# Kernel optimization log

Measured on AMD Instinct MI355X. Metric: run time of the kernel, lower is better.

## Reference

```python
import jax, jax.numpy as jnp
import numpy as np

N = 50000      # nodes
E = 800000     # edges (avg degree 16)
D_IN, D_H, D_OUT = 128, 128, 64


def setup_inputs() -> dict:
    key = jax.random.key(0)
    ks = jax.random.split(key, 12)
    s = 0.05  # weight init scale
    return {
        "x": jax.random.normal(ks[0], (N, D_IN), jnp.float32),
        "edge_index": jax.random.randint(ks[1], (2, E), 0, N, dtype=jnp.int64),
        "Wl0": jax.random.normal(ks[2], (D_H, D_IN), jnp.float32) * s,
        "bl0": jax.random.normal(ks[3], (D_H,), jnp.float32) * s,
        "Wr0": jax.random.normal(ks[4], (D_H, D_IN), jnp.float32) * s,
        "Wl1": jax.random.normal(ks[5], (D_H, D_H), jnp.float32) * s,
        "bl1": jax.random.normal(ks[6], (D_H,), jnp.float32) * s,
        "Wr1": jax.random.normal(ks[7], (D_H, D_H), jnp.float32) * s,
        "Wl2": jax.random.normal(ks[8], (D_OUT, D_H), jnp.float32) * s,
        "bl2": jax.random.normal(ks[9], (D_OUT,), jnp.float32) * s,
        "Wr2": jax.random.normal(ks[10], (D_OUT, D_H), jnp.float32) * s,
    }


def _sage_layer(h, src, dst, Wl, bl, Wr):
    # mean aggregation over incoming neighbors: out[i] = mean_{j in N(i)} h[j]
    n = h.shape[0]
    agg = jax.ops.segment_sum(h[src], dst, num_segments=n)          # [N, D]
    deg = jax.ops.segment_sum(jnp.ones((src.shape[0],), h.dtype), dst,
                              num_segments=n)                        # [N]
    mean = agg / jnp.maximum(deg, 1.0)[:, None]  # empty rows -> 0, matches torch_sparse
    # lin_l(agg) + lin_r(self); lin_r has no bias in PyG SAGEConv
    return mean @ Wl.T + bl + h @ Wr.T


def reference(x, edge_index, Wl0, bl0, Wr0, Wl1, bl1, Wr1, Wl2, bl2, Wr2):
    src, dst = edge_index[1], edge_index[0]  # adj row = dst, col = src
    h = jax.nn.relu(_sage_layer(x, src, dst, Wl0, bl0, Wr0))
    h = jax.nn.relu(_sage_layer(h, src, dst, Wl1, bl1, Wr1))
    h = _sage_layer(h, src, dst, Wl2, bl2, Wr2)
    return jax.nn.log_softmax(h, axis=1)
```

## Files before the change

kernel.cpp:

```cpp
#include <hip/hip_runtime.h>
#include <hip/hip_bf16.h>


typedef __attribute__((ext_vector_type(8))) short bf16x8;
typedef __attribute__((ext_vector_type(4))) float f32x4;

#define NPB 128
#define BCAP 2560
#define EPB 8192
#define EPT 32
#define CPAD 16

__device__ __forceinline__ unsigned short f2bf(float f) {
    unsigned int u = __builtin_bit_cast(unsigned int, f);
    u += 0x7fffu + ((u >> 16) & 1u);
    return (unsigned short)(u >> 16);
}
__device__ __forceinline__ float bf2f(unsigned int bits16) {
    return __builtin_bit_cast(float, bits16 << 16);
}


__global__ __launch_bounds__(256) void dist_cast_kernel(
        const int* __restrict__ dst, const int* __restrict__ srcv,
        int* __restrict__ gcnt, unsigned int* __restrict__ staging, int E, int NBc,
        const float* __restrict__ x,
        const float* p0, const float* p1, const float* p2,
        const float* p3, const float* p4, const float* p5,
        unsigned short* __restrict__ xbf, unsigned short* __restrict__ wbf,
        int xpairs, int distBlocks) {
    __shared__ unsigned int stage[EPB];
    __shared__ int hist[400];
    __shared__ int lstart[400];
    __shared__ int gbase[400];
    __shared__ int scanbuf[256];
    int t = threadIdx.x;

    if (blockIdx.x >= distBlocks) {
        int bid = blockIdx.x - distBlocks;
        int xblocks = (xpairs + 255) / 256;
        if (bid < xblocks) {
            int i = bid * 256 + t;
            if (i < xpairs) {
                float2 v = ((const float2*)x)[i];
                unsigned int p = (unsigned int)f2bf(v.x) | ((unsigned int)f2bf(v.y) << 16);
                ((unsigned int*)xbf)[i] = p;
            }
        } else {
            int w = (bid - xblocks) * 256 + t;
            if (w < 40960) {
                const float* src;
                int local;
                if      (w < 8192)  { src = p0; local = w; }
                else if (w < 16384) { src = p1; local = w - 8192; }
                else if (w < 24576) { src = p2; local = w - 16384; }
                else if (w < 32768) { src = p3; local = w - 24576; }
                else if (w < 36864) { src = p4; local = w - 32768; }
                else                { src = p5; local = w - 36864; }
                float2 v = ((const float2*)src)[local];
                unsigned int p = (unsigned int)f2bf(v.x) | ((unsigned int)f2bf(v.y) << 16);
                ((unsigned int*)wbf)[w] = p;
            }
        }
        return;
    }

    int e0 = blockIdx.x * EPB;
    unsigned int w[EPT];

    for (int b = t; b < NBc + 1; b += 256) hist[b] = 0;
    __syncthreads();

#pragma unroll
    for (int i = 0; i < EPT; ++i) {
        int e = e0 + i * 256 + t;
        unsigned int word = 0xFFFFFFFFu;
        if (e < E) word = ((unsigned int)dst[e] << 16) | (unsigned int)srcv[e];
        w[i] = word;
        int b = (int)(word >> 23); if (b > NBc) b = NBc;
        atomicAdd(&hist[b], 1);
    }
    __syncthreads();

    int b0 = 2 * t, b1 = 2 * t + 1;
    int h0 = (b0 <= NBc) ? hist[b0] : 0;
    int h1 = (b1 <= NBc) ? hist[b1] : 0;
    int pair = h0 + h1;
    scanbuf[t] = pair;
    __syncthreads();
    for (int off = 1; off < 256; off <<= 1) {
        int v = (t >= off) ? scanbuf[t - off] : 0;
        __syncthreads();
        scanbuf[t] += v;
        __syncthreads();
    }
    int excl = scanbuf[t] - pair;
    if (b0 <= NBc) lstart[b0] = excl;
    if (b1 <= NBc) lstart[b1] = excl + h0;
    __syncthreads();

    for (int b = t; b < NBc; b += 256) {
        int h = hist[b];
        gbase[b] = h ? atomicAdd(&gcnt[b * CPAD], h) : 0;
    }
    for (int b = t; b < NBc + 1; b += 256) hist[b] = lstart[b];
    __syncthreads();

#pragma unroll
    for (int i = 0; i < EPT; ++i) {
        unsigned int word = w[i];
        int b = (int)(word >> 23); if (b > NBc) b = NBc;
        int p = atomicAdd(&hist[b], 1);
        stage[p] = word;
    }
    __syncthreads();

    int total = lstart[NBc];
    for (int i = t; i < total; i += 256) {
        unsigned int word = stage[i];
        int b = (int)(word >> 23);
        int gpos = gbase[b] + (i - lstart[b]);
        staging[(size_t)b * BCAP + gpos] = word;
    }
}


__global__ __launch_bounds__(256) void build_kernel(const unsigned int* __restrict__ staging,
                                                    const int* __restrict__ gcnt,
                                                    int* __restrict__ row_ptr,
                                                    int* __restrict__ adj, int N, int NBc) {
    __shared__ int lstart[400];
    __shared__ int scanbuf[256];
    __shared__ int hist[NPB];
    __shared__ int scn[NPB];
    int b = blockIdx.x;
    int t = threadIdx.x;

    int b0 = 2 * t, b1 = 2 * t + 1;
    int h0 = (b0 < NBc) ? gcnt[b0 * CPAD] : 0;
    int h1 = (b1 < NBc) ? gcnt[b1 * CPAD] : 0;
    int pair = h0 + h1;
    scanbuf[t] = pair;
    __syncthreads();
    for (int off = 1; off < 256; off <<= 1) {
        int v = (t >= off) ? scanbuf[t - off] : 0;
        __syncthreads();
        scanbuf[t] += v;
        __syncthreads();
    }
    int excl = scanbuf[t] - pair;
    if (b0 < NBc) lstart[b0] = excl;
    if (b1 < NBc) lstart[b1] = excl + h0;
    if (b == 0 && t == 255) row_ptr[N] = scanbuf[255];
    __syncthreads();

    int n0 = b * NPB;
    int nb = N - n0; if (nb > NPB) nb = NPB;
    int ec = gcnt[b * CPAD];
    int bb = lstart[b];
    const unsigned int* st = staging + (size_t)b * BCAP;

    if (t < NPB) hist[t] = 0;
    __syncthreads();
    for (int i = t; i < ec; i += 256)
        atomicAdd(&hist[(st[i] >> 16) & (NPB - 1)], 1);
    __syncthreads();

    int v = (t < NPB) ? hist[t] : 0;
    if (t < NPB) scn[t] = v;
    __syncthreads();
    for (int off = 1; off < NPB; off <<= 1) {
        int u = (t >= off && t < NPB) ? scn[t - off] : 0;
        __syncthreads();
        if (t < NPB) scn[t] += u;
        __syncthreads();
    }
    if (t < NPB) hist[t] = scn[t] - v;
    if (t < nb) row_ptr[n0 + t] = bb + (scn[t] - v);
    __syncthreads();

    for (int i = t; i < ec; i += 256) {
        unsigned int pk = st[i];
        int p = atomicAdd(&hist[(pk >> 16) & (NPB - 1)], 1);
        adj[bb + p] = (int)(pk & 0xffffu);
    }
}


__global__ __launch_bounds__(256) void gemm_mfma_kernel(const unsigned short* __restrict__ H,
                                                        const unsigned short* __restrict__ Wl,
                                                        const unsigned short* __restrict__ Wr,
                                                        unsigned short* __restrict__ C,
                                                        int N, int ldC) {
    int wave = threadIdx.x >> 6;
    int lane = threadIdx.x & 63;
    int l15 = lane & 15, quad = lane >> 4;
    int y = blockIdx.y, half = gridDim.y >> 1;
    const unsigned short* W = (y < half) ? Wl : Wr;
    int wrow0 = (y < half ? y : y - half) * 64;
    int col0 = y * 64;
    int m0 = blockIdx.x * 128 + wave * 32;

    int r0 = m0 + l15;      if (r0 > N - 1) r0 = N - 1;
    int r1 = m0 + 16 + l15; if (r1 > N - 1) r1 = N - 1;
    const bf16x8* A0 = (const bf16x8*)(H + (size_t)r0 * 128);
    const bf16x8* A1 = (const bf16x8*)(H + (size_t)r1 * 128);

    f32x4 acc[2][4] = {};
#pragma unroll
    for (int ks = 0; ks < 4; ++ks) {
        int vidx = ks * 4 + quad;
        bf16x8 a0 = A0[vidx];
        bf16x8 a1 = A1[vidx];
#pragma unroll
        for (int j = 0; j < 4; ++j) {
            const bf16x8* B = (const bf16x8*)(W + (size_t)(wrow0 + j * 16 + l15) * 128);
            bf16x8 b = B[vidx];
            acc[0][j] = __builtin_amdgcn_mfma_f32_16x16x32_bf16(a0, b, acc[0][j], 0, 0, 0);
            acc[1][j] = __builtin_amdgcn_mfma_f32_16x16x32_bf16(a1, b, acc[1][j], 0, 0, 0);
        }
    }

#pragma unroll
    for (int i = 0; i < 2; ++i)
#pragma unroll
        for (int j = 0; j < 4; ++j)
#pragma unroll
            for (int r = 0; r < 4; ++r) {
                int row = m0 + i * 16 + quad * 4 + r;
                if (row < N) {
                    int col = col0 + j * 16 + l15;
                    C[(size_t)row * ldC + col] = f2bf(acc[i][j][r]);
                }
            }
}


__global__ __launch_bounds__(256) void agg_relu_kernel(const unsigned short* __restrict__ C,
                                                       const int* __restrict__ row_ptr,
                                                       const int* __restrict__ adj,
                                                       const float* __restrict__ bias,
                                                       unsigned short* __restrict__ hout, int N) {
    int node = (int)((blockIdx.x * blockDim.x + threadIdx.x) >> 6);
    int lane = threadIdx.x & 63;
    if (node >= N) return;
    int beg = row_ptr[node], end = row_ptr[node + 1];
    float sx[4] = {}, sy[4] = {};

    int e = beg;
    while (e < end) {
        int cnt = end - e; if (cnt > 64) cnt = 64;
        int c1 = cnt - 1;
        int ll = lane > c1 ? c1 : lane;
        int myidx = adj[e + ll];

        for (int i = 0; i < cnt; i += 16) {
            int rem = cnt - i;
            unsigned int v[16];
#pragma unroll
            for (int j = 0; j < 16; ++j) {
                int tt = i + j; if (tt > c1) tt = c1;
                int s = __shfl(myidx, tt);
                v[j] = ((const unsigned int*)(C + (size_t)s * 256))[lane];
            }
#pragma unroll
            for (int j = 0; j < 16; ++j) {
                float m = (j < rem) ? 1.f : 0.f;
                sx[j & 3] += m * bf2f(v[j] & 0xffffu);
                sy[j & 3] += m * bf2f(v[j] >> 16);
            }
        }
        e += cnt;
    }

    float fx = (sx[0] + sx[1]) + (sx[2] + sx[3]);
    float fy = (sy[0] + sy[1]) + (sy[2] + sy[3]);
    int deg = end - beg;
    float inv = 1.0f / (float)(deg > 1 ? deg : 1);
    float2 bb = ((const float2*)bias)[lane];
    unsigned int rv = ((const unsigned int*)(C + (size_t)node * 256))[64 + lane];
    float ox = fmaxf(fx * inv + bb.x + bf2f(rv & 0xffffu), 0.f);
    float oy = fmaxf(fy * inv + bb.y + bf2f(rv >> 16), 0.f);
    unsigned int p = (unsigned int)f2bf(ox) | ((unsigned int)f2bf(oy) << 16);
    ((unsigned int*)(hout + (size_t)node * 128))[lane] = p;
}


__global__ __launch_bounds__(256) void final_kernel(const unsigned short* __restrict__ C,
                                                    const int* __restrict__ row_ptr,
                                                    const int* __restrict__ adj,
                                                    const float* __restrict__ bias,
                                                    float* __restrict__ out, int N) {
    int node = (int)((blockIdx.x * blockDim.x + threadIdx.x) >> 6);
    int lane = threadIdx.x & 63;
    if (node >= N) return;
    int beg = row_ptr[node], end = row_ptr[node + 1];
    float a[4] = {};

    int e = beg;
    while (e < end) {
        int cnt = end - e; if (cnt > 64) cnt = 64;
        int c1 = cnt - 1;
        int ll = lane > c1 ? c1 : lane;
        int myidx = adj[e + ll];

        for (int i = 0; i < cnt; i += 16) {
            int rem = cnt - i;
            float v[16];
#pragma unroll
            for (int j = 0; j < 16; ++j) {
                int tt = i + j; if (tt > c1) tt = c1;
                int s = __shfl(myidx, tt);
                v[j] = bf2f((unsigned int)C[(size_t)s * 128 + lane]);
            }
#pragma unroll
            for (int j = 0; j < 16; ++j) {
                float m = (j < rem) ? 1.f : 0.f;
                a[j & 3] += m * v[j];
            }
        }
        e += cnt;
    }

    float sum = (a[0] + a[1]) + (a[2] + a[3]);
    int deg = end - beg;
    float inv = 1.0f / (float)(deg > 1 ? deg : 1);
    float u = sum * inv + bias[lane] + bf2f((unsigned int)C[(size_t)node * 128 + 64 + lane]);

    float m = u;
#pragma unroll
    for (int off = 32; off > 0; off >>= 1) m = fmaxf(m, __shfl_xor(m, off));
    float ex = __expf(u - m);
    float se = ex;
#pragma unroll
    for (int off = 32; off > 0; off >>= 1) se += __shfl_xor(se, off);
    out[(size_t)node * 64 + lane] = (u - m) - __logf(se);
}


extern "C" void kernel_launch(void* const* d_in, const int* in_sizes, int n_in,
                              void* d_out, int out_size, void* d_ws, size_t ws_size,
                              hipStream_t stream) {
    const float* x   = (const float*)d_in[0];
    const int*   ei  = (const int*)d_in[1];
    const float* Wl0 = (const float*)d_in[2];
    const float* bl0 = (const float*)d_in[3];
    const float* Wr0 = (const float*)d_in[4];
    const float* Wl1 = (const float*)d_in[5];
    const float* bl1 = (const float*)d_in[6];
    const float* Wr1 = (const float*)d_in[7];
    const float* Wl2 = (const float*)d_in[8];
    const float* bl2 = (const float*)d_in[9];
    const float* Wr2 = (const float*)d_in[10];
    float* out = (float*)d_out;

    const int N  = in_sizes[0] / 128;
    const int E  = in_sizes[1] / 2;
    const int NB = (N + NPB - 1) / NPB;

    char* ws = (char*)d_ws;
    auto alloc = [&](size_t bytes) {
        char* p = ws;
        ws += (bytes + 255) & ~(size_t)255;
        return p;
    };
    int*   row_ptr = (int*)alloc((size_t)(N + 1) * 4);
    int*   adj     = (int*)alloc((size_t)E * 4);
    int*   gcnt    = (int*)alloc((size_t)NB * CPAD * 4);
    unsigned int* staging = (unsigned int*)alloc((size_t)NB * BCAP * 4);
    unsigned short* xbf = (unsigned short*)alloc((size_t)N * 128 * 2);
    unsigned short* wbf = (unsigned short*)alloc((size_t)81920 * 2);
    unsigned short* C   = (unsigned short*)alloc((size_t)N * 256 * 2);
    unsigned short* hA  = (unsigned short*)alloc((size_t)N * 128 * 2);
    unsigned short* hB  = (unsigned short*)alloc((size_t)N * 128 * 2);

    const int* dstp = ei;
    const int* srcp = ei + E;

    hipMemsetAsync(gcnt, 0, (size_t)NB * CPAD * 4, stream);

    int distBlocks = (E + EPB - 1) / EPB;
    int xpairs = N * 64;
    int castBlocks = (xpairs + 255) / 256 + 160;
    dist_cast_kernel<<<distBlocks + castBlocks, 256, 0, stream>>>(
        dstp, srcp, gcnt, staging, E, NB,
        x, Wl0, Wr0, Wl1, Wr1, Wl2, Wr2, xbf, wbf, xpairs, distBlocks);

    build_kernel<<<NB, 256, 0, stream>>>(staging, gcnt, row_ptr, adj, N, NB);

    unsigned short* wl0 = wbf;
    unsigned short* wr0 = wbf + 16384;
    unsigned short* wl1 = wbf + 32768;
    unsigned short* wr1 = wbf + 49152;
    unsigned short* wl2 = wbf + 65536;
    unsigned short* wr2 = wbf + 73728;

    dim3 blk(256);
    int gemmRows = (N + 127) / 128;
    int aggBlocks = (N * 64 + 255) / 256;

    gemm_mfma_kernel<<<dim3(gemmRows, 4), blk, 0, stream>>>(xbf, wl0, wr0, C, N, 256);
    agg_relu_kernel<<<aggBlocks, blk, 0, stream>>>(C, row_ptr, adj, bl0, hA, N);
    gemm_mfma_kernel<<<dim3(gemmRows, 4), blk, 0, stream>>>(hA, wl1, wr1, C, N, 256);
    agg_relu_kernel<<<aggBlocks, blk, 0, stream>>>(C, row_ptr, adj, bl1, hB, N);
    gemm_mfma_kernel<<<dim3(gemmRows, 2), blk, 0, stream>>>(hB, wl2, wr2, C, N, 128);
    final_kernel<<<aggBlocks, blk, 0, stream>>>(C, row_ptr, adj, bl2, out, N);
}
```

Measured before the change: 281.5 us.

## Merge CSR build with first GEMM and split GEMM output into L/R buffers

The CSR build kernel and the layer-0 GEMM now run in one launch, with extra blocks doing GEMM tiles. Both depend only on outputs of the dist/cast kernel, so they can overlap, and one launch plus one dependency barrier is removed. The GEMM output is split into separate contiguous CL (neighbor projection) and CR (self projection) buffers. This makes the gathered rows in aggregation dense 256-byte rows instead of strided halves of 512-byte rows, so each cache line fetched holds only gathered data. The cost is a mixed-role kernel whose build blocks use shared memory that the GEMM blocks carry without using, which may lower occupancy.

```diff
diff --git a/kernel.cpp b/kernel.cpp
--- a/kernel.cpp
+++ b/kernel.cpp
@@ -125,81 +125,21 @@
 }
 
 
-__global__ __launch_bounds__(256) void build_kernel(const unsigned int* __restrict__ staging,
-                                                    const int* __restrict__ gcnt,
-                                                    int* __restrict__ row_ptr,
-                                                    int* __restrict__ adj, int N, int NBc) {
-    __shared__ int lstart[400];
-    __shared__ int scanbuf[256];
-    __shared__ int hist[NPB];
-    __shared__ int scn[NPB];
-    int b = blockIdx.x;
-    int t = threadIdx.x;
-
-    int b0 = 2 * t, b1 = 2 * t + 1;
-    int h0 = (b0 < NBc) ? gcnt[b0 * CPAD] : 0;
-    int h1 = (b1 < NBc) ? gcnt[b1 * CPAD] : 0;
-    int pair = h0 + h1;
-    scanbuf[t] = pair;
-    __syncthreads();
-    for (int off = 1; off < 256; off <<= 1) {
-        int v = (t >= off) ? scanbuf[t - off] : 0;
-        __syncthreads();
-        scanbuf[t] += v;
-        __syncthreads();
-    }
-    int excl = scanbuf[t] - pair;
-    if (b0 < NBc) lstart[b0] = excl;
-    if (b1 < NBc) lstart[b1] = excl + h0;
-    if (b == 0 && t == 255) row_ptr[N] = scanbuf[255];
-    __syncthreads();
-
-    int n0 = b * NPB;
-    int nb = N - n0; if (nb > NPB) nb = NPB;
-    int ec = gcnt[b * CPAD];
-    int bb = lstart[b];
-    const unsigned int* st = staging + (size_t)b * BCAP;
-
-    if (t < NPB) hist[t] = 0;
-    __syncthreads();
-    for (int i = t; i < ec; i += 256)
-        atomicAdd(&hist[(st[i] >> 16) & (NPB - 1)], 1);
-    __syncthreads();
-
-    int v = (t < NPB) ? hist[t] : 0;
-    if (t < NPB) scn[t] = v;
-    __syncthreads();
-    for (int off = 1; off < NPB; off <<= 1) {
-        int u = (t >= off && t < NPB) ? scn[t - off] : 0;
-        __syncthreads();
-        if (t < NPB) scn[t] += u;
-        __syncthreads();
-    }
-    if (t < NPB) hist[t] = scn[t] - v;
-    if (t < nb) row_ptr[n0 + t] = bb + (scn[t] - v);
-    __syncthreads();
-
-    for (int i = t; i < ec; i += 256) {
-        unsigned int pk = st[i];
-        int p = atomicAdd(&hist[(pk >> 16) & (NPB - 1)], 1);
-        adj[bb + p] = (int)(pk & 0xffffu);
-    }
-}
-
-
-__global__ __launch_bounds__(256) void gemm_mfma_kernel(const unsigned short* __restrict__ H,
-                                                        const unsigned short* __restrict__ Wl,
-                                                        const unsigned short* __restrict__ Wr,
-                                                        unsigned short* __restrict__ C,
-                                                        int N, int ldC) {
+__device__ __forceinline__ void gemm_tile(const unsigned short* __restrict__ H,
+                                          const unsigned short* __restrict__ Wl,
+                                          const unsigned short* __restrict__ Wr,
+                                          unsigned short* __restrict__ CL,
+                                          unsigned short* __restrict__ CR,
+                                          int bx, int y, int half, int ldC, int N) {
     int wave = threadIdx.x >> 6;
     int lane = threadIdx.x & 63;
     int l15 = lane & 15, quad = lane >> 4;
-    int y = blockIdx.y, half = gridDim.y >> 1;
     const unsigned short* W = (y < half) ? Wl : Wr;
-    int wrow0 = (y < half ? y : y - half) * 64;
-    int col0 = y * 64;
-    int m0 = blockIdx.x * 128 + wave * 32;
+    unsigned short* Cout = (y < half) ? CL : CR;
+    int slab = (y < half) ? y : y - half;
+    int wrow0 = slab * 64;
+    int col0 = slab * 64;
+    int m0 = bx * 128 + wave * 32;
 
     int r0 = m0 + l15;      if (r0 > N - 1) r0 = N - 1;
     int r1 = m0 + 16 + l15; if (r1 > N - 1) r1 = N - 1;
@@ -230,13 +170,94 @@
                 int row = m0 + i * 16 + quad * 4 + r;
                 if (row < N) {
                     int col = col0 + j * 16 + l15;
-                    C[(size_t)row * ldC + col] = f2bf(acc[i][j][r]);
+                    Cout[(size_t)row * ldC + col] = f2bf(acc[i][j][r]);
                 }
             }
 }
 
-
-__global__ __launch_bounds__(256) void agg_relu_kernel(const unsigned short* __restrict__ C,
+__global__ __launch_bounds__(256) void gemm_kernel(const unsigned short* __restrict__ H,
+                                                   const unsigned short* __restrict__ Wl,
+                                                   const unsigned short* __restrict__ Wr,
+                                                   unsigned short* __restrict__ CL,
+                                                   unsigned short* __restrict__ CR,
+                                                   int half, int ldC, int N) {
+    gemm_tile(H, Wl, Wr, CL, CR, blockIdx.x, blockIdx.y, half, ldC, N);
+}
+
+
+__global__ __launch_bounds__(256) void build_gemm0_kernel(
+        const unsigned int* __restrict__ staging, const int* __restrict__ gcnt,
+        int* __restrict__ row_ptr, int* __restrict__ adj, int N, int NBc,
+        const unsigned short* __restrict__ xbf,
+        const unsigned short* __restrict__ wl0, const unsigned short* __restrict__ wr0,
+        unsigned short* __restrict__ CL, unsigned short* __restrict__ CR,
+        int gemmRows) {
+    __shared__ int lstart[400];
+    __shared__ int scanbuf[256];
+    __shared__ int hist[NPB];
+    __shared__ int scn[NPB];
+    int t = threadIdx.x;
+
+    if (blockIdx.x >= (unsigned)NBc) {
+        int g = blockIdx.x - NBc;
+        gemm_tile(xbf, wl0, wr0, CL, CR, g % gemmRows, g / gemmRows, 2, 128, N);
+        return;
+    }
+    int b = blockIdx.x;
+
+    int b0 = 2 * t, b1 = 2 * t + 1;
+    int h0 = (b0 < NBc) ? gcnt[b0 * CPAD] : 0;
+    int h1 = (b1 < NBc) ? gcnt[b1 * CPAD] : 0;
+    int pair = h0 + h1;
+    scanbuf[t] = pair;
+    __syncthreads();
+    for (int off = 1; off < 256; off <<= 1) {
+        int v = (t >= off) ? scanbuf[t - off] : 0;
+        __syncthreads();
+        scanbuf[t] += v;
+        __syncthreads();
+    }
+    int excl = scanbuf[t] - pair;
+    if (b0 < NBc) lstart[b0] = excl;
+    if (b1 < NBc) lstart[b1] = excl + h0;
+    if (b == 0 && t == 255) row_ptr[N] = scanbuf[255];
+    __syncthreads();
+
+    int n0 = b * NPB;
+    int nb = N - n0; if (nb > NPB) nb = NPB;
+    int ec = gcnt[b * CPAD];
+    int bb = lstart[b];
+    const unsigned int* st = staging + (size_t)b * BCAP;
+
+    if (t < NPB) hist[t] = 0;
+    __syncthreads();
+    for (int i = t; i < ec; i += 256)
+        atomicAdd(&hist[(st[i] >> 16) & (NPB - 1)], 1);
+    __syncthreads();
+
+    int v = (t < NPB) ? hist[t] : 0;
+    if (t < NPB) scn[t] = v;
+    __syncthreads();
+    for (int off = 1; off < NPB; off <<= 1) {
+        int u = (t >= off && t < NPB) ? scn[t - off] : 0;
+        __syncthreads();
+        if (t < NPB) scn[t] += u;
+        __syncthreads();
+    }
+    if (t < NPB) hist[t] = scn[t] - v;
+    if (t < nb) row_ptr[n0 + t] = bb + (scn[t] - v);
+    __syncthreads();
+
+    for (int i = t; i < ec; i += 256) {
+        unsigned int pk = st[i];
+        int p = atomicAdd(&hist[(pk >> 16) & (NPB - 1)], 1);
+        adj[bb + p] = (int)(pk & 0xffffu);
+    }
+}
+
+
+__global__ __launch_bounds__(256) void agg_relu_kernel(const unsigned short* __restrict__ CL,
+                                                       const unsigned short* __restrict__ CR,
                                                        const int* __restrict__ row_ptr,
                                                        const int* __restrict__ adj,
                                                        const float* __restrict__ bias,
@@ -261,7 +282,7 @@
             for (int j = 0; j < 16; ++j) {
                 int tt = i + j; if (tt > c1) tt = c1;
                 int s = __shfl(myidx, tt);
-                v[j] = ((const unsigned int*)(C + (size_t)s * 256))[lane];
+                v[j] = ((const unsigned int*)(CL + (size_t)s * 128))[lane];
             }
 #pragma unroll
             for (int j = 0; j < 16; ++j) {
@@ -278,7 +299,7 @@
     int deg = end - beg;
     float inv = 1.0f / (float)(deg > 1 ? deg : 1);
     float2 bb = ((const float2*)bias)[lane];
-    unsigned int rv = ((const unsigned int*)(C + (size_t)node * 256))[64 + lane];
+    unsigned int rv = ((const unsigned int*)(CR + (size_t)node * 128))[lane];
     float ox = fmaxf(fx * inv + bb.x + bf2f(rv & 0xffffu), 0.f);
     float oy = fmaxf(fy * inv + bb.y + bf2f(rv >> 16), 0.f);
     unsigned int p = (unsigned int)f2bf(ox) | ((unsigned int)f2bf(oy) << 16);
@@ -286,7 +307,8 @@
 }
 
 
-__global__ __launch_bounds__(256) void final_kernel(const unsigned short* __restrict__ C,
+__global__ __launch_bounds__(256) void final_kernel(const unsigned short* __restrict__ CL,
+                                                    const unsigned short* __restrict__ CR,
                                                     const int* __restrict__ row_ptr,
                                                     const int* __restrict__ adj,
                                                     const float* __restrict__ bias,
@@ -311,7 +333,7 @@
             for (int j = 0; j < 16; ++j) {
                 int tt = i + j; if (tt > c1) tt = c1;
                 int s = __shfl(myidx, tt);
-                v[j] = bf2f((unsigned int)C[(size_t)s * 128 + lane]);
+                v[j] = bf2f((unsigned int)CL[(size_t)s * 64 + lane]);
             }
 #pragma unroll
             for (int j = 0; j < 16; ++j) {
@@ -325,7 +347,7 @@
     float sum = (a[0] + a[1]) + (a[2] + a[3]);
     int deg = end - beg;
     float inv = 1.0f / (float)(deg > 1 ? deg : 1);
-    float u = sum * inv + bias[lane] + bf2f((unsigned int)C[(size_t)node * 128 + 64 + lane]);
+    float u = sum * inv + bias[lane] + bf2f((unsigned int)CR[(size_t)node * 64 + lane]);
 
     float m = u;
 #pragma unroll
@@ -370,7 +392,8 @@
     unsigned int* staging = (unsigned int*)alloc((size_t)NB * BCAP * 4);
     unsigned short* xbf = (unsigned short*)alloc((size_t)N * 128 * 2);
     unsigned short* wbf = (unsigned short*)alloc((size_t)81920 * 2);
-    unsigned short* C   = (unsigned short*)alloc((size_t)N * 256 * 2);
+    unsigned short* CLb = (unsigned short*)alloc((size_t)N * 128 * 2);
+    unsigned short* CRb = (unsigned short*)alloc((size_t)N * 128 * 2);
     unsigned short* hA  = (unsigned short*)alloc((size_t)N * 128 * 2);
     unsigned short* hB  = (unsigned short*)alloc((size_t)N * 128 * 2);
 
@@ -386,8 +409,6 @@
         dstp, srcp, gcnt, staging, E, NB,
         x, Wl0, Wr0, Wl1, Wr1, Wl2, Wr2, xbf, wbf, xpairs, distBlocks);
 
-    build_kernel<<<NB, 256, 0, stream>>>(staging, gcnt, row_ptr, adj, N, NB);
-
     unsigned short* wl0 = wbf;
     unsigned short* wr0 = wbf + 16384;
     unsigned short* wl1 = wbf + 32768;
@@ -399,10 +420,12 @@
     int gemmRows = (N + 127) / 128;
     int aggBlocks = (N * 64 + 255) / 256;
 
-    gemm_mfma_kernel<<<dim3(gemmRows, 4), blk, 0, stream>>>(xbf, wl0, wr0, C, N, 256);
-    agg_relu_kernel<<<aggBlocks, blk, 0, stream>>>(C, row_ptr, adj, bl0, hA, N);
-    gemm_mfma_kernel<<<dim3(gemmRows, 4), blk, 0, stream>>>(hA, wl1, wr1, C, N, 256);
-    agg_relu_kernel<<<aggBlocks, blk, 0, stream>>>(C, row_ptr, adj, bl1, hB, N);
-    gemm_mfma_kernel<<<dim3(gemmRows, 2), blk, 0, stream>>>(hB, wl2, wr2, C, N, 128);
-    final_kernel<<<aggBlocks, blk, 0, stream>>>(C, row_ptr, adj, bl2, out, N);
-}
+    build_gemm0_kernel<<<NB + gemmRows * 4, blk, 0, stream>>>(
+        staging, gcnt, row_ptr, adj, N, NB, xbf, wl0, wr0, CLb, CRb, gemmRows);
+
+    agg_relu_kernel<<<aggBlocks, blk, 0, stream>>>(CLb, CRb, row_ptr, adj, bl0, hA, N);
+    gemm_kernel<<<dim3(gemmRows, 4), blk, 0, stream>>>(hA, wl1, wr1, CLb, CRb, 2, 128, N);
+    agg_relu_kernel<<<aggBlocks, blk, 0, stream>>>(CLb, CRb, row_ptr, adj, bl1, hB, N);
+    gemm_kernel<<<dim3(gemmRows, 2), blk, 0, stream>>>(hB, wl2, wr2, CLb, CRb, 1, 64, N);
+    final_kernel<<<aggBlocks, blk, 0, stream>>>(CLb, CRb, row_ptr, adj, bl2, out, N);
+}
```

Result: no change. 278.2 us (-1.1%).
